# Optimization experiments

Hardware: AMD Instinct MI355X
Metric: run time of the kernel (lower is better)

The kernel has to match this reference:

```python
import jax, jax.numpy as jnp
import numpy as np

H_MODEL = 1024
N_HEADS = 16
N_KV_HEADS = 4
HEAD_DIM = 64
SLIDING_WINDOW = 512
B, S = 2, 2048
NEG_INF = -1e9


def rotate_half(x):
    half = x.shape[-1] // 2
    return jnp.concatenate([-x[..., half:], x[..., :half]], axis=-1)


def setup_inputs() -> dict:
    key = jax.random.key(0)
    ks = jax.random.split(key, 8)
    hidden_states = jax.random.normal(ks[0], (B, S, H_MODEL), dtype=jnp.float32)
    # RoPE tables (HF style): cos/sin of shape [1, S, head_dim]
    inv_freq = 1.0 / (10000.0 ** (jnp.arange(0, HEAD_DIM, 2, dtype=jnp.float32) / HEAD_DIM))
    pos = jnp.arange(S, dtype=jnp.float32)
    freqs = jnp.einsum('s,d->sd', pos, inv_freq)            # [S, D/2]
    emb = jnp.concatenate([freqs, freqs], axis=-1)          # [S, D]
    cos = jnp.cos(emb)[None]                                # [1, S, D]
    sin = jnp.sin(emb)[None]
    # additive causal + sliding-window mask [1,1,S,S]
    i = jnp.arange(S)[:, None]
    j = jnp.arange(S)[None, :]
    allowed = (j <= i) & (i - j < SLIDING_WINDOW)
    attention_mask = jnp.where(allowed, 0.0, NEG_INF).astype(jnp.float32)[None, None]
    # projection weights (torch Linear stores [out, in]; y = x @ W.T)
    std = 0.02
    Wq = jax.random.normal(ks[1], (N_HEADS * HEAD_DIM, H_MODEL), dtype=jnp.float32) * std
    Wk = jax.random.normal(ks[2], (N_KV_HEADS * HEAD_DIM, H_MODEL), dtype=jnp.float32) * std
    Wv = jax.random.normal(ks[3], (N_KV_HEADS * HEAD_DIM, H_MODEL), dtype=jnp.float32) * std
    Wo = jax.random.normal(ks[4], (H_MODEL, N_HEADS * HEAD_DIM), dtype=jnp.float32) * std
    return {"hidden_states": hidden_states, "cos": cos, "sin": sin,
            "attention_mask": attention_mask, "Wq": Wq, "Wk": Wk, "Wv": Wv, "Wo": Wo}


def reference(hidden_states, cos, sin, attention_mask, Wq, Wk, Wv, Wo):
    b, s, _ = hidden_states.shape
    G = N_HEADS // N_KV_HEADS
    scaling = HEAD_DIM ** -0.5
    # QKV projections -> [B, H, S, D]
    q = jnp.einsum('bsh,oh->bso', hidden_states, Wq).reshape(b, s, N_HEADS, HEAD_DIM).transpose(0, 2, 1, 3)
    k = jnp.einsum('bsh,oh->bso', hidden_states, Wk).reshape(b, s, N_KV_HEADS, HEAD_DIM).transpose(0, 2, 1, 3)
    v = jnp.einsum('bsh,oh->bso', hidden_states, Wv).reshape(b, s, N_KV_HEADS, HEAD_DIM).transpose(0, 2, 1, 3)
    # RoPE (cos/sin broadcast over head dim via unsqueeze(1))
    c = cos[:, None, :, :]
    sn = sin[:, None, :, :]
    q = q * c + rotate_half(q) * sn
    k = k * c + rotate_half(k) * sn
    # GQA eager attention: group query heads over kv heads
    qg = q.reshape(b, N_KV_HEADS, G, s, HEAD_DIM)
    scores = jnp.einsum('bkgqd,bkpd->bkgqp', qg, k) * scaling  # [B,Hkv,G,S,S]
    scores = scores + attention_mask[:, :, None, :, :]
    probs = jax.nn.softmax(scores.astype(jnp.float32), axis=-1).astype(q.dtype)
    out = jnp.einsum('bkgqp,bkpd->bkgqd', probs, v)            # [B,Hkv,G,S,D]
    out = out.reshape(b, N_HEADS, s, HEAD_DIM).transpose(0, 2, 1, 3).reshape(b, s, N_HEADS * HEAD_DIM)
    return jnp.einsum('bso,ho->bsh', out, Wo)
```

## Files before the change

### kernel.cpp

```cpp
#include <hip/hip_runtime.h>
#include <hip/hip_bf16.h>

#define S_LEN 2048
#define NH 16
#define NKV 4
#define HD 64
#define WIN 512
#define BATCH 2

typedef __bf16 bf16_8 __attribute__((ext_vector_type(8)));
typedef __bf16 bf16_4 __attribute__((ext_vector_type(4)));
typedef float f32x4 __attribute__((ext_vector_type(4)));

__global__ __launch_bounds__(256) void cvt5(
    const float* __restrict__ s0, const float* __restrict__ s1,
    const float* __restrict__ s2, const float* __restrict__ s3,
    const float* __restrict__ s4,
    __bf16* __restrict__ d0, __bf16* __restrict__ d1,
    __bf16* __restrict__ d2, __bf16* __restrict__ d3,
    __bf16* __restrict__ d4,
    int c0, int c1, int c2, int c3, int c4)
{
    const int i = blockIdx.x * blockDim.x + threadIdx.x;
    if (i >= c4) return;
    const float* s; __bf16* d; int base;
    if (i < c0)      { s = s0; d = d0; base = 0;  }
    else if (i < c1) { s = s1; d = d1; base = c0; }
    else if (i < c2) { s = s2; d = d2; base = c1; }
    else if (i < c3) { s = s3; d = d3; base = c2; }
    else             { s = s4; d = d4; base = c3; }
    const size_t j = (size_t)(i - base) * 4;
    const f32x4 v = *(const f32x4*)(s + j);
    bf16_4 o;
    o[0] = (__bf16)v[0]; o[1] = (__bf16)v[1];
    o[2] = (__bf16)v[2]; o[3] = (__bf16)v[3];
    *(bf16_4*)(d + j) = o;
}

#define GEMM_BODY(Aptr_, Bptr_, row0_, colb_)                                  \
    const int tid  = threadIdx.x;                                              \
    const int wave = tid >> 6;                                                 \
    const int lane = tid & 63;                                                 \
    const int wm   = wave & 1;                                                 \
    const int wn   = wave >> 1;                                                \
    __bf16* const As = smem;                                    \
    __bf16* const Bs = smem + 4608;                             \
    const int ar = tid >> 2, ac = (tid & 3) << 4;                              \
    const int br = tid >> 1, bc = (tid & 1) << 5;                              \
    const int fm = lane & 15;                                                  \
    const int fj = (lane >> 4) << 3;                                           \
    const f32x4 fzero = {0.f, 0.f, 0.f, 0.f};                                  \
    f32x4 acc[2][4];                                                           \
    _Pragma("unroll") for (int i = 0; i < 2; ++i)                              \
        _Pragma("unroll") for (int nt = 0; nt < 4; ++nt) acc[i][nt] = fzero;   \
    const size_t aoff = (size_t)(row0_ + ar) * 1024 + ac;                      \
    const size_t boff = (size_t)(colb_ + br) * 1024 + bc;                      \
    bf16_8 pa0 = *(const bf16_8*)&Aptr_[aoff];                                 \
    bf16_8 pa1 = *(const bf16_8*)&Aptr_[aoff + 8];                             \
    bf16_8 pb0 = *(const bf16_8*)&Bptr_[boff];                                 \
    bf16_8 pb1 = *(const bf16_8*)&Bptr_[boff + 8];                             \
    bf16_8 pb2 = *(const bf16_8*)&Bptr_[boff + 16];                            \
    bf16_8 pb3 = *(const bf16_8*)&Bptr_[boff + 24];                            \
    for (int it = 0; it < 16; ++it) {                                          \
        *(bf16_8*)&As[ar * 72 + ac]     = pa0;                                 \
        *(bf16_8*)&As[ar * 72 + ac + 8] = pa1;                                 \
        *(bf16_8*)&Bs[br * 72 + bc]      = pb0;                                \
        *(bf16_8*)&Bs[br * 72 + bc + 8]  = pb1;                                \
        *(bf16_8*)&Bs[br * 72 + bc + 16] = pb2;                                \
        *(bf16_8*)&Bs[br * 72 + bc + 24] = pb3;                                \
        __syncthreads();                                                       \
        if (it + 1 < 16) {                                                     \
            const int k0 = (it + 1) << 6;                                      \
            pa0 = *(const bf16_8*)&Aptr_[aoff + k0];                           \
            pa1 = *(const bf16_8*)&Aptr_[aoff + k0 + 8];                       \
            pb0 = *(const bf16_8*)&Bptr_[boff + k0];                           \
            pb1 = *(const bf16_8*)&Bptr_[boff + k0 + 8];                       \
            pb2 = *(const bf16_8*)&Bptr_[boff + k0 + 16];                      \
            pb3 = *(const bf16_8*)&Bptr_[boff + k0 + 24];                      \
        }                                                                      \
        _Pragma("unroll") for (int kk = 0; kk < 64; kk += 32) {                \
            bf16_8 af[2], bfr[4];                                              \
            _Pragma("unroll") for (int i = 0; i < 2; ++i)                      \
                af[i] = *(const bf16_8*)&As[(wm * 32 + i * 16 + fm) * 72 + kk + fj]; \
            _Pragma("unroll") for (int nt = 0; nt < 4; ++nt)                   \
                bfr[nt] = *(const bf16_8*)&Bs[(wn * 64 + nt * 16 + fm) * 72 + kk + fj]; \
            _Pragma("unroll") for (int i = 0; i < 2; ++i)                      \
                _Pragma("unroll") for (int nt = 0; nt < 4; ++nt)               \
                    acc[i][nt] = __builtin_amdgcn_mfma_f32_16x16x32_bf16(      \
                        af[i], bfr[nt], acc[i][nt], 0, 0, 0);                  \
        }                                                                      \
        __syncthreads();                                                       \
    }                                                                          \
    const int drow = (lane >> 4) << 2;

__global__ __launch_bounds__(256) void gemm_qkv(
    const __bf16* __restrict__ A,
    const __bf16* __restrict__ Wqb,
    const __bf16* __restrict__ Wkb,
    const __bf16* __restrict__ Wvb,
    __bf16* __restrict__ Qb,
    __bf16* __restrict__ Kb,
    __bf16* __restrict__ Vt,
    const float* __restrict__ cosb,
    const float* __restrict__ sinb)
{
    __shared__ __align__(16) __bf16 smem[13824];

    const int row0 = blockIdx.x * 64;
    const int by   = blockIdx.y;

    const __bf16* B; int colb; int mode;
    __bf16* C; int ldc; int col0;
    if (by < 8)       { B = Wqb; colb = by * 128;        C = Qb; ldc = 1024; col0 = by * 128;        mode = 0; }
    else if (by < 10) { B = Wkb; colb = (by - 8) * 128;  C = Kb; ldc = 256;  col0 = (by - 8) * 128;  mode = 1; }
    else              { B = Wvb; colb = (by - 10) * 128; C = 0;  ldc = 0;    col0 = (by - 10) * 128; mode = 2; }

    GEMM_BODY(A, B, row0, colb)

    const int cq = col0 + wn * 64;
    if (mode < 2) {
#pragma unroll
        for (int i = 0; i < 2; ++i) {
#pragma unroll
            for (int r = 0; r < 4; ++r) {
                const int row = row0 + wm * 32 + i * 16 + drow + r;
                const int s   = row & (S_LEN - 1);
#pragma unroll
                for (int nt = 0; nt < 2; ++nt) {
                    const int d = nt * 16 + fm;
                    const float c1 = cosb[s * HD + d];
                    const float s1 = sinb[s * HD + d];
                    const float c2 = cosb[s * HD + d + 32];
                    const float s2 = sinb[s * HD + d + 32];
                    const float x1 = acc[i][nt][r];
                    const float x2 = acc[i][nt + 2][r];
                    C[(size_t)row * ldc + cq + d]      = (__bf16)(x1 * c1 - x2 * s1);
                    C[(size_t)row * ldc + cq + d + 32] = (__bf16)(x2 * c2 + x1 * s2);
                }
            }
        }
    } else {
        __bf16* T = smem;
#pragma unroll
        for (int i = 0; i < 2; ++i)
#pragma unroll
            for (int r = 0; r < 4; ++r)
#pragma unroll
                for (int nt = 0; nt < 4; ++nt)
                    T[(wn * 64 + nt * 16 + fm) * 72 + wm * 32 + i * 16 + drow + r] =
                        (__bf16)acc[i][nt][r];
        __syncthreads();
        const int nl = tid >> 1;
        const int so = (tid & 1) << 5;
        const int ng = col0 + nl;
        const int kh = ng >> 6, d = ng & 63;
        const int b  = row0 >> 11, s0v = row0 & (S_LEN - 1);
        __bf16* dst = &Vt[(size_t)((b * NKV + kh) * HD + d) * S_LEN + s0v + so];
#pragma unroll
        for (int c = 0; c < 4; ++c)
            *(bf16_8*)(dst + c * 8) = *(const bf16_8*)&T[nl * 72 + so + c * 8];
    }
}

__global__ __launch_bounds__(256) void gemm_o(
    const __bf16* __restrict__ A,
    const __bf16* __restrict__ B,
    float* __restrict__ C)
{
    __shared__ __align__(16) __bf16 smem[13824];

    const int row0 = blockIdx.x * 64;
    const int colb = blockIdx.y * 128;

    GEMM_BODY(A, B, row0, colb)

#pragma unroll
    for (int i = 0; i < 2; ++i)
#pragma unroll
        for (int r = 0; r < 4; ++r) {
            const int row = row0 + wm * 32 + i * 16 + drow + r;
#pragma unroll
            for (int nt = 0; nt < 4; ++nt)
                C[(size_t)row * 1024 + colb + wn * 64 + nt * 16 + fm] = acc[i][nt][r];
        }
}

__global__ __launch_bounds__(256) void attn_mfma(const __bf16* __restrict__ Q,
                                                 const __bf16* __restrict__ K,
                                                 const __bf16* __restrict__ Vt,
                                                 __bf16* __restrict__ O)
{
    __shared__ __align__(16) __bf16 Ks[64 * 72];
    __shared__ __align__(16) __bf16 Vs[64 * 72];
    __shared__ __align__(16) __bf16 Ps[4][16][72];

    const int tid  = threadIdx.x;
    const int wave = tid >> 6;
    const int lane = tid & 63;

    const int qt = blockIdx.x & (S_LEN / 64 - 1);
    const int h  = (blockIdx.x >> 5) & (NH - 1);
    const int b  = blockIdx.x >> 9;
    const int kh = h >> 2;

    const int q0 = qt * 64;
    const int qw = q0 + wave * 16;

    const int fm = lane & 15;
    const int fj = (lane >> 4) << 3;

    const size_t qrow = (size_t)(b * S_LEN + qw + fm) * (NH * HD) + h * HD;
    const bf16_8 qf0 = *(const bf16_8*)&Q[qrow + fj];
    const bf16_8 qf1 = *(const bf16_8*)&Q[qrow + 32 + fj];

    const f32x4 fzero = {0.f, 0.f, 0.f, 0.f};
    f32x4 oacc[4];
    float l[4];
#pragma unroll
    for (int nt = 0; nt < 4; ++nt) oacc[nt] = fzero;
#pragma unroll
    for (int r = 0; r < 4; ++r) l[r] = 0.f;

    const int kr = tid >> 3;
    const int kc = (tid & 7) << 3;
    const size_t kbase = (size_t)(b * S_LEN + kr) * (NKV * HD) + kh * HD + kc;
    const size_t vbase = (size_t)((b * NKV + kh) * HD + kr) * S_LEN + kc;
    const int qbase = qw + ((lane >> 4) << 2);

    const int lo  = (q0 >= WIN) ? (q0 - WIN) : 0;
    const int nit = ((q0 - lo) >> 6) + 1;

    bf16_8 pk0 = *(const bf16_8*)&K[kbase + (size_t)lo * (NKV * HD)];
    bf16_8 pk1 = *(const bf16_8*)&K[kbase + (size_t)(lo + 32) * (NKV * HD)];
    bf16_8 pv0 = *(const bf16_8*)&Vt[vbase + lo];
    bf16_8 pv1 = *(const bf16_8*)&Vt[vbase + (size_t)32 * S_LEN + lo];

    for (int it = 0; it < nit; ++it) {
        const int kb = lo + (it << 6);
        *(bf16_8*)&Ks[kr * 72 + kc]        = pk0;
        *(bf16_8*)&Ks[(kr + 32) * 72 + kc] = pk1;
        *(bf16_8*)&Vs[kr * 72 + kc]        = pv0;
        *(bf16_8*)&Vs[(kr + 32) * 72 + kc] = pv1;
        __syncthreads();

        if (it + 1 < nit) {
            const int kn = kb + 64;
            pk0 = *(const bf16_8*)&K[kbase + (size_t)kn * (NKV * HD)];
            pk1 = *(const bf16_8*)&K[kbase + (size_t)(kn + 32) * (NKV * HD)];
            pv0 = *(const bf16_8*)&Vt[vbase + kn];
            pv1 = *(const bf16_8*)&Vt[vbase + (size_t)32 * S_LEN + kn];
        }

        if (kb <= qw + 15 && (qw - kb) < (WIN + 63)) {
            f32x4 sc[4];
#pragma unroll
            for (int t = 0; t < 4; ++t) {
                const bf16_8 klo = *(const bf16_8*)&Ks[(t * 16 + fm) * 72 + fj];
                const bf16_8 khi = *(const bf16_8*)&Ks[(t * 16 + fm) * 72 + 32 + fj];
                f32x4 s = fzero;
                s = __builtin_amdgcn_mfma_f32_16x16x32_bf16(qf0, klo, s, 0, 0, 0);
                s = __builtin_amdgcn_mfma_f32_16x16x32_bf16(qf1, khi, s, 0, 0, 0);
                sc[t] = s;
            }

#pragma unroll
            for (int t = 0; t < 4; ++t) {
                const int ki = kb + t * 16 + fm;
#pragma unroll
                for (int r = 0; r < 4; ++r) {
                    const int qr = qbase + r;
                    const float e = __expf(sc[t][r] * 0.125f);
                    const float p = (ki <= qr && qr - ki < WIN) ? e : 0.f;
                    l[r] += p;
                    Ps[wave][((lane >> 4) << 2) + r][t * 16 + fm] = (__bf16)p;
                }
            }

            const bf16_8 pf0 = *(const bf16_8*)&Ps[wave][fm][fj];
            const bf16_8 pf1 = *(const bf16_8*)&Ps[wave][fm][32 + fj];
#pragma unroll
            for (int nt = 0; nt < 4; ++nt) {
                const bf16_8 vlo = *(const bf16_8*)&Vs[(nt * 16 + fm) * 72 + fj];
                const bf16_8 vhi = *(const bf16_8*)&Vs[(nt * 16 + fm) * 72 + 32 + fj];
                oacc[nt] = __builtin_amdgcn_mfma_f32_16x16x32_bf16(pf0, vlo, oacc[nt], 0, 0, 0);
                oacc[nt] = __builtin_amdgcn_mfma_f32_16x16x32_bf16(pf1, vhi, oacc[nt], 0, 0, 0);
            }
        }
        __syncthreads();
    }

#pragma unroll
    for (int off = 8; off > 0; off >>= 1)
#pragma unroll
        for (int r = 0; r < 4; ++r)
            l[r] += __shfl_xor(l[r], off, 64);

    const int drow = (lane >> 4) << 2;
    float inv[4];
#pragma unroll
    for (int r = 0; r < 4; ++r) inv[r] = 1.0f / l[r];
#pragma unroll
    for (int nt = 0; nt < 4; ++nt)
#pragma unroll
        for (int r = 0; r < 4; ++r) {
            const size_t off = (size_t)(b * S_LEN + qw + drow + r) * (NH * HD) + h * HD + nt * 16 + fm;
            O[off] = (__bf16)(oacc[nt][r] * inv[r]);
        }
}

extern "C" void kernel_launch(void* const* d_in, const int* in_sizes, int n_in,
                              void* d_out, int out_size, void* d_ws, size_t ws_size,
                              hipStream_t stream)
{
    const float* hs   = (const float*)d_in[0];
    const float* cosb = (const float*)d_in[1];
    const float* sinb = (const float*)d_in[2];
    const float* Wq = (const float*)d_in[4];
    const float* Wk = (const float*)d_in[5];
    const float* Wv = (const float*)d_in[6];
    const float* Wo = (const float*)d_in[7];

    const int M = BATCH * S_LEN;

    __bf16* hsb = (__bf16*)d_ws;
    __bf16* Wqb = hsb + (size_t)M * 1024;
    __bf16* Wkb = Wqb + 1024 * 1024;
    __bf16* Wvb = Wkb + 256 * 1024;
    __bf16* Wob = Wvb + 256 * 1024;
    __bf16* Qb  = Wob + 1024 * 1024;
    __bf16* Kb  = Qb  + (size_t)M * 1024;
    __bf16* Vtb = Kb  + (size_t)M * 256;
    __bf16* Ob  = Vtb + (size_t)M * 256;

    const int c0 = 1048576;
    const int c1 = c0 + 262144;
    const int c2 = c1 + 65536;
    const int c3 = c2 + 65536;
    const int c4 = c3 + 262144;

    dim3 blk(256);
    cvt5<<<(c4 + 255) / 256, blk, 0, stream>>>(hs, Wq, Wk, Wv, Wo,
                                               hsb, Wqb, Wkb, Wvb, Wob,
                                               c0, c1, c2, c3, c4);

    gemm_qkv<<<dim3(64, 12), blk, 0, stream>>>(hsb, Wqb, Wkb, Wvb,
                                               Qb, Kb, Vtb, cosb, sinb);

    attn_mfma<<<BATCH * NH * (S_LEN / 64), blk, 0, stream>>>(Qb, Kb, Vtb, Ob);

    gemm_o<<<dim3(64, 8), blk, 0, stream>>>(Ob, Wob, (float*)d_out);
}
```

Before: 161.2 us.

## Pre-pack weights into MFMA fragment layout and load B directly to registers

The conversion kernel now writes the bf16 weights in a fragment-packed layout matching the 16x16x32 MFMA operand order. The GEMM kernels can then load B fragments straight from global memory into registers, skipping the LDS staging. The A tile is double-buffered in LDS with one barrier per iteration, and B loads are prefetched across the two k-halves. This removes LDS traffic and a sync per K-step, at the cost of uncoalesced-looking per-wave global loads that depend on L2 reuse across blocks.

```diff
diff --git a/kernel.cpp b/kernel.cpp
--- a/kernel.cpp
+++ b/kernel.cpp
@@ -12,41 +12,46 @@
 typedef __bf16 bf16_4 __attribute__((ext_vector_type(4)));
 typedef float f32x4 __attribute__((ext_vector_type(4)));
 
-__global__ __launch_bounds__(256) void cvt5(
-    const float* __restrict__ s0, const float* __restrict__ s1,
-    const float* __restrict__ s2, const float* __restrict__ s3,
-    const float* __restrict__ s4,
-    __bf16* __restrict__ d0, __bf16* __restrict__ d1,
-    __bf16* __restrict__ d2, __bf16* __restrict__ d3,
-    __bf16* __restrict__ d4,
-    int c0, int c1, int c2, int c3, int c4)
-{
-    const int i = blockIdx.x * blockDim.x + threadIdx.x;
-    if (i >= c4) return;
-    const float* s; __bf16* d; int base;
-    if (i < c0)      { s = s0; d = d0; base = 0;  }
-    else if (i < c1) { s = s1; d = d1; base = c0; }
-    else if (i < c2) { s = s2; d = d2; base = c1; }
-    else if (i < c3) { s = s3; d = d3; base = c2; }
-    else             { s = s4; d = d4; base = c3; }
-    const size_t j = (size_t)(i - base) * 4;
-    const f32x4 v = *(const f32x4*)(s + j);
-    bf16_4 o;
-    o[0] = (__bf16)v[0]; o[1] = (__bf16)v[1];
-    o[2] = (__bf16)v[2]; o[3] = (__bf16)v[3];
-    *(bf16_4*)(d + j) = o;
-}
-
-#define GEMM_BODY(Aptr_, Bptr_, row0_, colb_)                                  \
-    const int tid  = threadIdx.x;                                              \
-    const int wave = tid >> 6;                                                 \
-    const int lane = tid & 63;                                                 \
-    const int wm   = wave & 1;                                                 \
-    const int wn   = wave >> 1;                                                \
-    __bf16* const As = smem;                                    \
-    __bf16* const Bs = smem + 4608;                             \
+__device__ inline bf16_8 cvt8(f32x4 a, f32x4 b) {
+    bf16_8 r;
+    r[0] = (__bf16)a[0]; r[1] = (__bf16)a[1]; r[2] = (__bf16)a[2]; r[3] = (__bf16)a[3];
+    r[4] = (__bf16)b[0]; r[5] = (__bf16)b[1]; r[6] = (__bf16)b[2]; r[7] = (__bf16)b[3];
+    return r;
+}
+
+__global__ __launch_bounds__(256) void cvt_pack(
+    const float* __restrict__ hs, const float* __restrict__ Wq,
+    const float* __restrict__ Wk, const float* __restrict__ Wv,
+    const float* __restrict__ Wo,
+    __bf16* __restrict__ hsb, __bf16* __restrict__ Wqp,
+    __bf16* __restrict__ Wkp, __bf16* __restrict__ Wvp,
+    __bf16* __restrict__ Wop)
+{
+    int i = blockIdx.x * 256 + threadIdx.x;
+    if (i < 524288) {
+        const size_t j = (size_t)i * 8;
+        const f32x4 a = *(const f32x4*)(hs + j);
+        const f32x4 b = *(const f32x4*)(hs + j + 4);
+        *(bf16_8*)(hsb + j) = cvt8(a, b);
+        return;
+    }
+    i -= 524288;
+    const float* S; __bf16* P;
+    if (i < 131072)      { S = Wq; P = Wqp; }
+    else if (i < 163840) { S = Wk; P = Wkp; i -= 131072; }
+    else if (i < 196608) { S = Wv; P = Wvp; i -= 163840; }
+    else                 { S = Wo; P = Wop; i -= 196608; }
+    const int n = i >> 7;
+    const int k = (i & 127) << 3;
+    const f32x4 a = *(const f32x4*)(S + (size_t)n * 1024 + k);
+    const f32x4 b = *(const f32x4*)(S + (size_t)n * 1024 + k + 4);
+    const size_t dst = ((size_t)((n >> 4) * 32 + (k >> 5)) << 9)
+                     + ((size_t)((n & 15) | (((k >> 3) & 3) << 4)) << 3);
+    *(bf16_8*)(P + dst) = cvt8(a, b);
+}
+
+#define GEMM_K_LOOP(Ap_, Bq_, row0_)                                           \
     const int ar = tid >> 2, ac = (tid & 3) << 4;                              \
-    const int br = tid >> 1, bc = (tid & 1) << 5;                              \
     const int fm = lane & 15;                                                  \
     const int fj = (lane >> 4) << 3;                                           \
     const f32x4 fzero = {0.f, 0.f, 0.f, 0.f};                                  \
@@ -54,40 +59,49 @@
     _Pragma("unroll") for (int i = 0; i < 2; ++i)                              \
         _Pragma("unroll") for (int nt = 0; nt < 4; ++nt) acc[i][nt] = fzero;   \
     const size_t aoff = (size_t)(row0_ + ar) * 1024 + ac;                      \
-    const size_t boff = (size_t)(colb_ + br) * 1024 + bc;                      \
-    bf16_8 pa0 = *(const bf16_8*)&Aptr_[aoff];                                 \
-    bf16_8 pa1 = *(const bf16_8*)&Aptr_[aoff + 8];                             \
-    bf16_8 pb0 = *(const bf16_8*)&Bptr_[boff];                                 \
-    bf16_8 pb1 = *(const bf16_8*)&Bptr_[boff + 8];                             \
-    bf16_8 pb2 = *(const bf16_8*)&Bptr_[boff + 16];                            \
-    bf16_8 pb3 = *(const bf16_8*)&Bptr_[boff + 24];                            \
+    bf16_8 b0[4], b1[4];                                                       \
+    {                                                                          \
+        const bf16_8 a0 = *(const bf16_8*)&Ap_[aoff];                          \
+        const bf16_8 a1 = *(const bf16_8*)&Ap_[aoff + 8];                      \
+        *(bf16_8*)&As[ar * 72 + ac]     = a0;                                  \
+        *(bf16_8*)&As[ar * 72 + ac + 8] = a1;                                  \
+        _Pragma("unroll") for (int nt = 0; nt < 4; ++nt)                       \
+            b0[nt] = *(const bf16_8*)(Bq_ + nt * 16384);                       \
+    }                                                                          \
+    __syncthreads();                                                           \
     for (int it = 0; it < 16; ++it) {                                          \
-        *(bf16_8*)&As[ar * 72 + ac]     = pa0;                                 \
-        *(bf16_8*)&As[ar * 72 + ac + 8] = pa1;                                 \
-        *(bf16_8*)&Bs[br * 72 + bc]      = pb0;                                \
-        *(bf16_8*)&Bs[br * 72 + bc + 8]  = pb1;                                \
-        *(bf16_8*)&Bs[br * 72 + bc + 16] = pb2;                                \
-        *(bf16_8*)&Bs[br * 72 + bc + 24] = pb3;                                \
-        __syncthreads();                                                       \
-        if (it + 1 < 16) {                                                     \
-            const int k0 = (it + 1) << 6;                                      \
-            pa0 = *(const bf16_8*)&Aptr_[aoff + k0];                           \
-            pa1 = *(const bf16_8*)&Aptr_[aoff + k0 + 8];                       \
-            pb0 = *(const bf16_8*)&Bptr_[boff + k0];                           \
-            pb1 = *(const bf16_8*)&Bptr_[boff + k0 + 8];                       \
-            pb2 = *(const bf16_8*)&Bptr_[boff + k0 + 16];                      \
-            pb3 = *(const bf16_8*)&Bptr_[boff + k0 + 24];                      \
+        const int cur = it & 1;                                                \
+        const bool pf = it < 15;                                               \
+        bf16_8 qa0, qa1, bn[4];                                                \
+        if (pf) {                                                              \
+            qa0 = *(const bf16_8*)&Ap_[aoff + (it + 1) * 64];                  \
+            qa1 = *(const bf16_8*)&Ap_[aoff + (it + 1) * 64 + 8];              \
         }                                                                      \
-        _Pragma("unroll") for (int kk = 0; kk < 64; kk += 32) {                \
-            bf16_8 af[2], bfr[4];                                              \
-            _Pragma("unroll") for (int i = 0; i < 2; ++i)                      \
-                af[i] = *(const bf16_8*)&As[(wm * 32 + i * 16 + fm) * 72 + kk + fj]; \
+        _Pragma("unroll") for (int nt = 0; nt < 4; ++nt)                       \
+            b1[nt] = *(const bf16_8*)(Bq_ + nt * 16384 + (it * 2 + 1) * 512);  \
+        bf16_8 af0[2];                                                         \
+        _Pragma("unroll") for (int i = 0; i < 2; ++i)                          \
+            af0[i] = *(const bf16_8*)&As[cur * 4608 + (wm * 32 + i * 16 + fm) * 72 + fj]; \
+        _Pragma("unroll") for (int i = 0; i < 2; ++i)                          \
             _Pragma("unroll") for (int nt = 0; nt < 4; ++nt)                   \
-                bfr[nt] = *(const bf16_8*)&Bs[(wn * 64 + nt * 16 + fm) * 72 + kk + fj]; \
-            _Pragma("unroll") for (int i = 0; i < 2; ++i)                      \
-                _Pragma("unroll") for (int nt = 0; nt < 4; ++nt)               \
-                    acc[i][nt] = __builtin_amdgcn_mfma_f32_16x16x32_bf16(      \
-                        af[i], bfr[nt], acc[i][nt], 0, 0, 0);                  \
+                acc[i][nt] = __builtin_amdgcn_mfma_f32_16x16x32_bf16(          \
+                    af0[i], b0[nt], acc[i][nt], 0, 0, 0);                      \
+        if (pf) {                                                              \
+            _Pragma("unroll") for (int nt = 0; nt < 4; ++nt)                   \
+                bn[nt] = *(const bf16_8*)(Bq_ + nt * 16384 + (it + 1) * 1024); \
+        }                                                                      \
+        bf16_8 af1[2];                                                         \
+        _Pragma("unroll") for (int i = 0; i < 2; ++i)                          \
+            af1[i] = *(const bf16_8*)&As[cur * 4608 + (wm * 32 + i * 16 + fm) * 72 + 32 + fj]; \
+        _Pragma("unroll") for (int i = 0; i < 2; ++i)                          \
+            _Pragma("unroll") for (int nt = 0; nt < 4; ++nt)                   \
+                acc[i][nt] = __builtin_amdgcn_mfma_f32_16x16x32_bf16(          \
+                    af1[i], b1[nt], acc[i][nt], 0, 0, 0);                      \
+        if (pf) {                                                              \
+            const int nb = cur ^ 1;                                            \
+            *(bf16_8*)&As[nb * 4608 + ar * 72 + ac]     = qa0;                 \
+            *(bf16_8*)&As[nb * 4608 + ar * 72 + ac + 8] = qa1;                 \
+            _Pragma("unroll") for (int nt = 0; nt < 4; ++nt) b0[nt] = bn[nt];  \
         }                                                                      \
         __syncthreads();                                                       \
     }                                                                          \
@@ -95,27 +109,36 @@
 
 __global__ __launch_bounds__(256) void gemm_qkv(
     const __bf16* __restrict__ A,
-    const __bf16* __restrict__ Wqb,
-    const __bf16* __restrict__ Wkb,
-    const __bf16* __restrict__ Wvb,
+    const __bf16* __restrict__ Wqp,
+    const __bf16* __restrict__ Wkp,
+    const __bf16* __restrict__ Wvp,
     __bf16* __restrict__ Qb,
     __bf16* __restrict__ Kb,
     __bf16* __restrict__ Vt,
     const float* __restrict__ cosb,
     const float* __restrict__ sinb)
 {
-    __shared__ __align__(16) __bf16 smem[13824];
+    __shared__ __align__(16) __bf16 smem[9216];
+    __bf16* const As = smem;
+
+    const int tid  = threadIdx.x;
+    const int wave = tid >> 6;
+    const int lane = tid & 63;
+    const int wm   = wave & 1;
+    const int wn   = wave >> 1;
 
     const int row0 = blockIdx.x * 64;
     const int by   = blockIdx.y;
 
-    const __bf16* B; int colb; int mode;
+    const __bf16* Bp; int colb; int mode;
     __bf16* C; int ldc; int col0;
-    if (by < 8)       { B = Wqb; colb = by * 128;        C = Qb; ldc = 1024; col0 = by * 128;        mode = 0; }
-    else if (by < 10) { B = Wkb; colb = (by - 8) * 128;  C = Kb; ldc = 256;  col0 = (by - 8) * 128;  mode = 1; }
-    else              { B = Wvb; colb = (by - 10) * 128; C = 0;  ldc = 0;    col0 = (by - 10) * 128; mode = 2; }
-
-    GEMM_BODY(A, B, row0, colb)
+    if (by < 8)       { Bp = Wqp; colb = by * 128;        C = Qb; ldc = 1024; col0 = by * 128;        mode = 0; }
+    else if (by < 10) { Bp = Wkp; colb = (by - 8) * 128;  C = Kb; ldc = 256;  col0 = (by - 8) * 128;  mode = 1; }
+    else              { Bp = Wvp; colb = (by - 10) * 128; C = 0;  ldc = 0;    col0 = (by - 10) * 128; mode = 2; }
+
+    const __bf16* Bq = Bp + (size_t)((colb + wn * 64) >> 4) * 16384 + (lane << 3);
+
+    GEMM_K_LOOP(A, Bq, row0)
 
     const int cq = col0 + wn * 64;
     if (mode < 2) {
@@ -164,15 +187,24 @@
 
 __global__ __launch_bounds__(256) void gemm_o(
     const __bf16* __restrict__ A,
-    const __bf16* __restrict__ B,
+    const __bf16* __restrict__ Bp,
     float* __restrict__ C)
 {
-    __shared__ __align__(16) __bf16 smem[13824];
+    __shared__ __align__(16) __bf16 smem[9216];
+    __bf16* const As = smem;
+
+    const int tid  = threadIdx.x;
+    const int wave = tid >> 6;
+    const int lane = tid & 63;
+    const int wm   = wave & 1;
+    const int wn   = wave >> 1;
 
     const int row0 = blockIdx.x * 64;
     const int colb = blockIdx.y * 128;
 
-    GEMM_BODY(A, B, row0, colb)
+    const __bf16* Bq = Bp + (size_t)((colb + wn * 64) >> 4) * 16384 + (lane << 3);
+
+    GEMM_K_LOOP(A, Bq, row0)
 
 #pragma unroll
     for (int i = 0; i < 2; ++i)
@@ -323,30 +355,23 @@
     const int M = BATCH * S_LEN;
 
     __bf16* hsb = (__bf16*)d_ws;
-    __bf16* Wqb = hsb + (size_t)M * 1024;
-    __bf16* Wkb = Wqb + 1024 * 1024;
-    __bf16* Wvb = Wkb + 256 * 1024;
-    __bf16* Wob = Wvb + 256 * 1024;
-    __bf16* Qb  = Wob + 1024 * 1024;
+    __bf16* Wqp = hsb + (size_t)M * 1024;
+    __bf16* Wkp = Wqp + 1024 * 1024;
+    __bf16* Wvp = Wkp + 256 * 1024;
+    __bf16* Wop = Wvp + 256 * 1024;
+    __bf16* Qb  = Wop + 1024 * 1024;
     __bf16* Kb  = Qb  + (size_t)M * 1024;
     __bf16* Vtb = Kb  + (size_t)M * 256;
     __bf16* Ob  = Vtb + (size_t)M * 256;
 
-    const int c0 = 1048576;
-    const int c1 = c0 + 262144;
-    const int c2 = c1 + 65536;
-    const int c3 = c2 + 65536;
-    const int c4 = c3 + 262144;
-
     dim3 blk(256);
-    cvt5<<<(c4 + 255) / 256, blk, 0, stream>>>(hs, Wq, Wk, Wv, Wo,
-                                               hsb, Wqb, Wkb, Wvb, Wob,
-                                               c0, c1, c2, c3, c4);
-
-    gemm_qkv<<<dim3(64, 12), blk, 0, stream>>>(hsb, Wqb, Wkb, Wvb,
+    cvt_pack<<<3328, blk, 0, stream>>>(hs, Wq, Wk, Wv, Wo,
+                                       hsb, Wqp, Wkp, Wvp, Wop);
+
+    gemm_qkv<<<dim3(64, 12), blk, 0, stream>>>(hsb, Wqp, Wkp, Wvp,
                                                Qb, Kb, Vtb, cosb, sinb);
 
     attn_mfma<<<BATCH * NH * (S_LEN / 64), blk, 0, stream>>>(Qb, Kb, Vtb, Ob);
 
-    gemm_o<<<dim3(64, 8), blk, 0, stream>>>(Ob, Wob, (float*)d_out);
-}
+    gemm_o<<<dim3(64, 8), blk, 0, stream>>>(Ob, Wop, (float*)d_out);
+}
```

After: 160.6 us. Within noise of the previous version (-0.4%).
